# Kernel optimization log

Hardware: AMD Instinct MI355X
Metric: run time of the kernel (lower is better)

Reference implementation:

```python
import jax, jax.numpy as jnp
import numpy as np

B, C, N, T = 16, 32, 300, 12
ST, DH, CO = 40, 16, 32
DY_INTERVAL = 3
GDEP = 2
ALPHA = 0.05


def setup_inputs() -> dict:
    key = jax.random.key(0)
    ks = jax.random.split(key, 12)
    w = lambda k, shape, s=0.1: (jax.random.normal(k, shape, jnp.float32) * s)
    return {
        "x": jax.random.normal(ks[0], (B, C, N, T), jnp.float32),
        "st_node_fea": jax.random.normal(ks[1], (N, ST), jnp.float32),
        "W_s2d": w(ks[2], (ST, DH)), "b_s2d": jnp.zeros((DH,), jnp.float32),
        "W_rz": w(ks[3], (C + DH, 2 * DH)), "b_rz": jnp.zeros((2 * DH,), jnp.float32),
        "W_h": w(ks[4], (C + DH, DH)), "b_h": jnp.zeros((DH,), jnp.float32),
        "W_c1_fc2": w(ks[5], (2 * DH, DH)), "b_c1_fc2": jnp.zeros((DH,), jnp.float32),
        "W_c1_fc1": w(ks[6], (DH, 1)), "b_c1_fc1": jnp.zeros((1,), jnp.float32),
        "W_c2_fc2": w(ks[7], (2 * DH, DH)), "b_c2_fc2": jnp.zeros((DH,), jnp.float32),
        "W_c2_fc1": w(ks[8], (DH, 1)), "b_c2_fc1": jnp.zeros((1,), jnp.float32),
        "W_mlp": w(ks[9], ((GDEP + 1) * C, CO)), "b_mlp": jnp.zeros((CO,), jnp.float32),
    }


def _edge_score(hs, W_fc2, b_fc2, W_fc1, b_fc1):
    # normal_conv: fc1(relu(fc2(concat([sent, revi], -1)))).
    # fc2 over concat is decomposed into two halves to avoid the [B,N,N,2*DH] concat.
    dh = hs.shape[-1]
    Wa, Wb = W_fc2[:dh], W_fc2[dh:]
    h = jax.nn.relu((hs @ Wa)[:, :, None, :] + (hs @ Wb)[:, None, :, :] + b_fc2)  # [B,N,N,DH]
    return (h @ W_fc1 + b_fc1)[..., 0]  # [B,N,N]


def reference(x, st_node_fea, W_s2d, b_s2d, W_rz, b_rz, W_h, b_h,
              W_c1_fc2, b_c1_fc2, W_c1_fc1, b_c1_fc1,
              W_c2_fc2, b_c2_fc2, W_c2_fc1, b_c2_fc1, W_mlp, b_mlp):
    b, c, n, t = x.shape
    nc = t // DY_INTERVAL
    states0 = jnp.broadcast_to((st_node_fea @ W_s2d + b_s2d)[None], (b, n, DH)) + 0.0
    chunks = jnp.moveaxis(x.reshape(b, c, n, nc, DY_INTERVAL), 3, 0)  # [nc,B,C,N,di]

    def step(states, x_i):
        # GRU-style dynamic graph learner
        inp = jnp.mean(x_i, axis=-1).transpose(0, 2, 1)  # [B,N,C]
        cat = jnp.concatenate([inp, states], -1)
        rz = jax.nn.sigmoid(cat @ W_rz + b_rz)
        r, z = jnp.split(rz, 2, axis=-1)
        h_ = jnp.tanh(jnp.concatenate([inp, r * states], -1) @ W_h + b_h)
        new_state = z * states + (1.0 - z) * h_
        hs = jax.nn.relu(new_state)  # [B,N,DH]
        support = _edge_score(hs, W_c1_fc2, b_c1_fc2, W_c1_fc1, b_c1_fc1)
        mask = _edge_score(hs, W_c2_fc2, b_c2_fc2, W_c2_fc1, b_c2_fc1)
        adj = support * jax.nn.sigmoid(mask)  # [B,N,N]
        # MixProp multi-hop graph conv
        h = x_i
        outs = [h]
        for _ in range(GDEP):
            h = ALPHA * x_i + (1.0 - ALPHA) * jnp.einsum('bcwt,bvw->bcvt', h, adj)
            outs.append(h)
        ho = jnp.concatenate(outs, axis=1)  # [B,(GDEP+1)*C,N,di]
        out = jnp.einsum('bcnt,co->bont', ho, W_mlp) + b_mlp[None, :, None, None]
        return new_state, out

    _, outs = jax.lax.scan(step, states0, chunks)  # [nc,B,CO,N,di]
    return jnp.moveaxis(outs, 0, 3).reshape(b, W_mlp.shape[1], n, t)
```

## Files before the change

kernel.cpp:

```cpp
#include <hip/hip_runtime.h>
#include <hip/hip_bf16.h>
#include <math.h>

#define BB 16
#define CC 32
#define NN 300
#define TT 12
#define STF 40
#define DHD 16
#define COO 32
#define NCH 4
#define COL 96
#define NIB 64
#define KP  320
#define ALPHAF 0.05f

typedef __attribute__((ext_vector_type(8))) short short8;
typedef __attribute__((ext_vector_type(4))) float f32x4;

#define O_INP   0
#define O_XT    614400
#define O_GA1   2457600
#define O_GB1   2764800
#define O_GA2   3072000
#define O_GB2   3379200
#define O_ADJB  3686400
#define O_XTB   6963200
#define O_H1B   7946240

__device__ __forceinline__ float sigf(float x){ return 1.0f/(1.0f+expf(-x)); }

__global__ void k_prep(const float* __restrict__ x, float* __restrict__ xt,
                       __hip_bfloat16* __restrict__ xtb, float* __restrict__ inp){
    int idx = blockIdx.x*256 + threadIdx.x;
    if (idx >= BB*CC*NN) return;
    int n = idx % NN;
    int c = (idx / NN) % CC;
    int b = idx / (NN*CC);
    const float* xp = x + ((b*CC + c)*NN + n)*TT;
    float v[TT];
    #pragma unroll
    for (int t=0;t<TT;t++) v[t] = xp[t];
    #pragma unroll
    for (int i=0;i<NCH;i++){
        float m = (v[3*i]+v[3*i+1]+v[3*i+2])*(1.0f/3.0f);
        int ib = i*BB + b;
        inp[((size_t)ib*NN + n)*CC + c] = m;
        #pragma unroll
        for (int t=0;t<3;t++){
            float val = v[3*i+t];
            int col = c*3 + t;
            xt [((size_t)ib*NN + n)*COL + col] = val;
            xtb[((size_t)ib*COL + col)*KP + n] = __float2bfloat16(val);
        }
    }
}

__global__ void k_gru_all(const float* __restrict__ stnf, const float* __restrict__ W_s2d,
                          const float* __restrict__ b_s2d, const float* __restrict__ inp,
                          const float* __restrict__ W_rz, const float* __restrict__ b_rz,
                          const float* __restrict__ W_h,  const float* __restrict__ b_h,
                          const float* __restrict__ Wc1,  const float* __restrict__ Wc2,
                          float* __restrict__ ga1, float* __restrict__ gb1,
                          float* __restrict__ ga2, float* __restrict__ gb2){
    int row = blockIdx.x;
    int n   = row % NN;
    int tid = threadIdx.x;
    __shared__ float cat[48];
    __shared__ float r_s[16], z_s[16], hs_s[16], st_s[16];
    if (tid < 16){
        float acc = b_s2d[tid];
        const float* srow = stnf + n*STF;
        #pragma unroll
        for (int k=0;k<STF;k++) acc += srow[k]*W_s2d[k*DHD + tid];
        st_s[tid] = acc;
    }
    __syncthreads();
    for (int i=0;i<NCH;i++){
        const float* ip = inp + ((size_t)i*BB*NN + row)*CC;
        if (tid < CC) cat[tid] = ip[tid];
        else if (tid < 48) cat[tid] = st_s[tid-32];
        __syncthreads();
        if (tid < 32){
            float acc = b_rz[tid];
            #pragma unroll
            for (int k=0;k<48;k++) acc += cat[k]*W_rz[k*32 + tid];
            float s = sigf(acc);
            if (tid < 16) r_s[tid] = s; else z_s[tid-16] = s;
        }
        __syncthreads();
        if (tid < 16) cat[32+tid] = r_s[tid]*st_s[tid];
        __syncthreads();
        if (tid < 16){
            float acc = b_h[tid];
            #pragma unroll
            for (int k=0;k<48;k++) acc += cat[k]*W_h[k*DHD + tid];
            float h_ = tanhf(acc);
            float z  = z_s[tid];
            float ns = z*st_s[tid] + (1.0f-z)*h_;
            st_s[tid] = ns;
            hs_s[tid] = fmaxf(ns, 0.0f);
        }
        __syncthreads();
        int j = tid & 15, which = tid >> 4;
        const float* W = (which < 2) ? Wc1 : Wc2;
        int off = (which & 1) ? 16*DHD : 0;
        float acc = 0.0f;
        #pragma unroll
        for (int k=0;k<16;k++) acc += hs_s[k]*W[off + k*DHD + j];
        float* dst = (which==0)? ga1 : (which==1)? gb1 : (which==2)? ga2 : gb2;
        dst[((size_t)i*BB*NN + row)*DHD + j] = acc;
        __syncthreads();
    }
}

#define AVT 8
__global__ void k_adj(const float* __restrict__ ga1, const float* __restrict__ gb1,
                      const float* __restrict__ ga2, const float* __restrict__ gb2,
                      const float* __restrict__ bfc2_1, const float* __restrict__ wfc1_1, const float* __restrict__ bfc1_1,
                      const float* __restrict__ bfc2_2, const float* __restrict__ wfc1_2, const float* __restrict__ bfc1_2,
                      __hip_bfloat16* __restrict__ adjb){
    int tile = blockIdx.x % 38;
    int ib   = blockIdx.x / 38;
    int v0 = tile * AVT;
    int tid = threadIdx.x;
    __shared__ float a1[AVT][16], a2[AVT][16];
    __shared__ float w1[16], w2[16];
    if (tid < 16) w1[tid] = wfc1_1[tid];
    else if (tid < 32) w2[tid-16] = wfc1_2[tid-16];
    {
        int vl = tid >> 5, which = (tid >> 4) & 1, k = tid & 15;
        int v = v0 + vl;
        float val = 0.0f;
        if (v < NN)
            val = which ? (ga2[((size_t)ib*NN+v)*DHD + k] + bfc2_2[k])
                        : (ga1[((size_t)ib*NN+v)*DHD + k] + bfc2_1[k]);
        if (which) a2[vl][k] = val; else a1[vl][k] = val;
    }
    float B1 = bfc1_1[0], B2 = bfc1_2[0];
    __syncthreads();
    for (int w = tid; w < KP; w += 256){
        if (w < NN){
            const float4* p1 = (const float4*)(gb1 + ((size_t)ib*NN + w)*DHD);
            const float4* p2 = (const float4*)(gb2 + ((size_t)ib*NN + w)*DHD);
            float4 A[4], Bv[4];
            #pragma unroll
            for (int q=0;q<4;q++){ A[q]=p1[q]; Bv[q]=p2[q]; }
            const float* g1 = (const float*)A;
            const float* g2 = (const float*)Bv;
            for (int vl=0; vl<AVT; vl++){
                if (v0+vl >= NN) break;
                float s = B1, m = B2;
                #pragma unroll
                for (int k=0;k<16;k++){
                    s += fmaxf(a1[vl][k] + g1[k], 0.0f)*w1[k];
                    m += fmaxf(a2[vl][k] + g2[k], 0.0f)*w2[k];
                }
                adjb[((size_t)ib*KP + v0+vl)*KP + w] = __float2bfloat16(s * sigf(m));
            }
        } else {
            for (int vl=0; vl<AVT; vl++){
                if (v0+vl >= NN) break;
                adjb[((size_t)ib*KP + v0+vl)*KP + w] = __float2bfloat16(0.0f);
            }
        }
    }
}

__device__ __forceinline__ void conv_mfma_tile(const __hip_bfloat16* __restrict__ adjb,
                                               const __hip_bfloat16* __restrict__ Hb,
                                               int ib, int v0, int wave, int lane,
                                               f32x4& acc0, f32x4& acc1, f32x4& acc2){
    int l15 = lane & 15, lk = lane >> 4;
    int wrow = (wave & 1) * 16;
    int wcol = (wave >> 1) * 48;
    const short8* Ap  = (const short8*)(adjb + ((size_t)ib*KP + v0 + wrow + l15)*KP + 8*lk);
    const short8* Bp0 = (const short8*)(Hb   + ((size_t)ib*COL + wcol +  0 + l15)*KP + 8*lk);
    const short8* Bp1 = (const short8*)(Hb   + ((size_t)ib*COL + wcol + 16 + l15)*KP + 8*lk);
    const short8* Bp2 = (const short8*)(Hb   + ((size_t)ib*COL + wcol + 32 + l15)*KP + 8*lk);
    #pragma unroll 2
    for (int kk=0; kk<KP/32; kk++){
        short8 a = Ap[kk*4];
        acc0 = __builtin_amdgcn_mfma_f32_16x16x32_bf16(a, Bp0[kk*4], acc0, 0, 0, 0);
        acc1 = __builtin_amdgcn_mfma_f32_16x16x32_bf16(a, Bp1[kk*4], acc1, 0, 0, 0);
        acc2 = __builtin_amdgcn_mfma_f32_16x16x32_bf16(a, Bp2[kk*4], acc2, 0, 0, 0);
    }
}

__global__ __launch_bounds__(256) void k_conv1(const __hip_bfloat16* __restrict__ adjb,
                                               const __hip_bfloat16* __restrict__ xtb,
                                               const float* __restrict__ xt,
                                               __hip_bfloat16* __restrict__ h1b){
    int ib = blockIdx.x / 10;
    int v0 = (blockIdx.x % 10) * 32;
    int tid = threadIdx.x;
    int wave = tid >> 6, lane = tid & 63;
    int l15 = lane & 15, lk = lane >> 4;
    int wrow = (wave & 1) * 16;
    int wcol = (wave >> 1) * 48;
    __shared__ float hbuf[COL][33];
    f32x4 acc0 = {0.f,0.f,0.f,0.f}, acc1 = acc0, acc2 = acc0;
    conv_mfma_tile(adjb, xtb, ib, v0, wave, lane, acc0, acc1, acc2);
    f32x4 accs[3] = {acc0, acc1, acc2};
    #pragma unroll
    for (int t=0;t<3;t++){
        int col = wcol + t*16 + l15;
        #pragma unroll
        for (int r=0;r<4;r++){
            int vloc = wrow + lk*4 + r;
            int v = v0 + vloc;
            float xval = (v < NN) ? xt[((size_t)ib*NN + v)*COL + col] : 0.0f;
            hbuf[col][vloc] = ALPHAF*xval + (1.0f-ALPHAF)*accs[t][r];
        }
    }
    __syncthreads();
    for (int idx = tid; idx < COL*32; idx += 256){
        int col = idx >> 5, vloc = idx & 31;
        int v = v0 + vloc;
        if (v < NN)
            h1b[((size_t)ib*COL + col)*KP + v] = __float2bfloat16(hbuf[col][vloc]);
    }
}

__global__ __launch_bounds__(256) void k_conv2_mlp(const __hip_bfloat16* __restrict__ adjb,
                                                   const __hip_bfloat16* __restrict__ h1b,
                                                   const float* __restrict__ xt,
                                                   const float* __restrict__ Wm,
                                                   const float* __restrict__ bmlp,
                                                   float* __restrict__ out){
    int ib = blockIdx.x / 10;
    int v0 = (blockIdx.x % 10) * 32;
    int b  = ib % BB, chunk = ib / BB;
    int tid = threadIdx.x;
    int wave = tid >> 6, lane = tid & 63;
    int l15 = lane & 15, lk = lane >> 4;
    int wrow = (wave & 1) * 16;
    int wcol = (wave >> 1) * 48;
    __shared__ float hs[3][COL][33];
    f32x4 acc0 = {0.f,0.f,0.f,0.f}, acc1 = acc0, acc2 = acc0;
    conv_mfma_tile(adjb, h1b, ib, v0, wave, lane, acc0, acc1, acc2);
    f32x4 accs[3] = {acc0, acc1, acc2};
    #pragma unroll
    for (int t=0;t<3;t++){
        int col = wcol + t*16 + l15;
        #pragma unroll
        for (int r=0;r<4;r++){
            int vloc = wrow + lk*4 + r;
            int v = v0 + vloc;
            float xval = (v < NN) ? xt[((size_t)ib*NN + v)*COL + col] : 0.0f;
            hs[2][col][vloc] = ALPHAF*xval + (1.0f-ALPHAF)*accs[t][r];
        }
    }
    for (int idx = tid; idx < 32*COL; idx += 256){
        int vloc = idx / COL, col = idx % COL;
        int v = v0 + vloc;
        hs[0][col][vloc] = (v < NN) ? xt[((size_t)ib*NN + v)*COL + col] : 0.0f;
    }
    for (int idx = tid; idx < COL*32; idx += 256){
        int col = idx >> 5, vloc = idx & 31;
        int v = v0 + vloc;
        hs[1][col][vloc] = (v < NN) ? __bfloat162float(h1b[((size_t)ib*COL + col)*KP + v]) : 0.0f;
    }
    __syncthreads();
    for (int e = tid; e < COO*32*3; e += 256){
        int o  = e / 96;
        int r  = e % 96;
        int vl = r / 3, t = r % 3;
        int v = v0 + vl;
        if (v >= NN) continue;
        float acc = bmlp[o];
        #pragma unroll
        for (int c=0;c<CC;c++){
            int col = c*3 + t;
            acc += hs[0][col][vl]*Wm[c*COO + o]
                 + hs[1][col][vl]*Wm[(CC+c)*COO + o]
                 + hs[2][col][vl]*Wm[(2*CC+c)*COO + o];
        }
        out[(((size_t)b*COO + o)*NN + v)*TT + chunk*3 + t] = acc;
    }
}

extern "C" void kernel_launch(void* const* d_in, const int* in_sizes, int n_in,
                              void* d_out, int out_size, void* d_ws, size_t ws_size,
                              hipStream_t stream){
    const float* x     = (const float*)d_in[0];
    const float* stnf  = (const float*)d_in[1];
    const float* W_s2d = (const float*)d_in[2];
    const float* b_s2d = (const float*)d_in[3];
    const float* W_rz  = (const float*)d_in[4];
    const float* b_rz  = (const float*)d_in[5];
    const float* W_h   = (const float*)d_in[6];
    const float* b_h   = (const float*)d_in[7];
    const float* Wc1f2 = (const float*)d_in[8];
    const float* bc1f2 = (const float*)d_in[9];
    const float* Wc1f1 = (const float*)d_in[10];
    const float* bc1f1 = (const float*)d_in[11];
    const float* Wc2f2 = (const float*)d_in[12];
    const float* bc2f2 = (const float*)d_in[13];
    const float* Wc2f1 = (const float*)d_in[14];
    const float* bc2f1 = (const float*)d_in[15];
    const float* W_mlp = (const float*)d_in[16];
    const float* b_mlp = (const float*)d_in[17];
    float* out = (float*)d_out;
    float* ws  = (float*)d_ws;

    float* inp = ws + O_INP;
    float* xt  = ws + O_XT;
    float* ga1 = ws + O_GA1;
    float* gb1 = ws + O_GB1;
    float* ga2 = ws + O_GA2;
    float* gb2 = ws + O_GB2;
    __hip_bfloat16* adjb = (__hip_bfloat16*)(ws + O_ADJB);
    __hip_bfloat16* xtb  = (__hip_bfloat16*)(ws + O_XTB);
    __hip_bfloat16* h1b  = (__hip_bfloat16*)(ws + O_H1B);

    hipLaunchKernelGGL(k_prep, dim3(600), dim3(256), 0, stream, x, xt, xtb, inp);
    hipLaunchKernelGGL(k_gru_all, dim3(BB*NN), dim3(64), 0, stream,
                       stnf, W_s2d, b_s2d, inp, W_rz, b_rz, W_h, b_h, Wc1f2, Wc2f2,
                       ga1, gb1, ga2, gb2);
    hipLaunchKernelGGL(k_adj, dim3(NIB*38), dim3(256), 0, stream,
                       ga1, gb1, ga2, gb2,
                       bc1f2, Wc1f1, bc1f1, bc2f2, Wc2f1, bc2f1, adjb);
    hipLaunchKernelGGL(k_conv1, dim3(NIB*10), dim3(256), 0, stream,
                       adjb, xtb, xt, h1b);
    hipLaunchKernelGGL(k_conv2_mlp, dim3(NIB*10), dim3(256), 0, stream,
                       adjb, h1b, xt, W_mlp, b_mlp, out);
}
```

Baseline: 255.0 us.

## Run the MixProp MLP on bf16 MFMA and store x/h1 as bf16

Replaces the scalar fp32 MLP loop in k_conv2_mlp with bf16 16x16x32 MFMA tiles. It reads x, h1 and a transposed bf16 W_mlp staged in LDS in a [t][hop][v][c] layout. The fp32 xt buffer becomes a bf16 node-major copy, and conv1 also writes a node-major h1 copy so conv2 can load it with coalesced reads. k_prep now zero-fills the KP padding of xtb and h1b. The aim is lower ALU time and less memory traffic, at the cost of extra bf16 rounding on the x and MLP inputs.

```diff
diff --git a/kernel.cpp b/kernel.cpp
--- a/kernel.cpp
+++ b/kernel.cpp
@@ -14,26 +14,44 @@
 #define NIB 64
 #define KP  320
 #define ALPHAF 0.05f
+#define HS 40
 
 typedef __attribute__((ext_vector_type(8))) short short8;
 typedef __attribute__((ext_vector_type(4))) float f32x4;
+typedef unsigned short ushort_t;
 
 #define O_INP   0
-#define O_XT    614400
-#define O_GA1   2457600
-#define O_GB1   2764800
-#define O_GA2   3072000
-#define O_GB2   3379200
-#define O_ADJB  3686400
-#define O_XTB   6963200
-#define O_H1B   7946240
+#define O_XVB   614400
+#define O_GA1   1536000
+#define O_GB1   1843200
+#define O_GA2   2150400
+#define O_GB2   2457600
+#define O_ADJB  2764800
+#define O_XTB   6041600
+#define O_H1B   7024640
+#define O_H1VB  8007680
+#define O_WMB   8929280
 
 __device__ __forceinline__ float sigf(float x){ return 1.0f/(1.0f+expf(-x)); }
 
-__global__ void k_prep(const float* __restrict__ x, float* __restrict__ xt,
-                       __hip_bfloat16* __restrict__ xtb, float* __restrict__ inp){
+__global__ void k_prep(const float* __restrict__ x, __hip_bfloat16* __restrict__ xtb,
+                       __hip_bfloat16* __restrict__ xvb, float* __restrict__ inp,
+                       __hip_bfloat16* __restrict__ h1b, const float* __restrict__ Wm,
+                       __hip_bfloat16* __restrict__ Wmb){
     int idx = blockIdx.x*256 + threadIdx.x;
     if (idx >= BB*CC*NN) return;
+    if (idx < NIB*COL*(KP-NN)){
+        int kk  = idx % (KP-NN);
+        int col = (idx / (KP-NN)) % COL;
+        int ib  = idx / ((KP-NN)*COL);
+        size_t off = ((size_t)ib*COL + col)*KP + NN + kk;
+        xtb[off] = __float2bfloat16(0.0f);
+        h1b[off] = __float2bfloat16(0.0f);
+    }
+    if (idx < COO*COL){
+        int o = idx / COL, k = idx % COL;
+        Wmb[o*COL + k] = __float2bfloat16(Wm[k*COO + o]);
+    }
     int n = idx % NN;
     int c = (idx / NN) % CC;
     int b = idx / (NN*CC);
@@ -50,8 +68,8 @@
         for (int t=0;t<3;t++){
             float val = v[3*i+t];
             int col = c*3 + t;
-            xt [((size_t)ib*NN + n)*COL + col] = val;
             xtb[((size_t)ib*COL + col)*KP + n] = __float2bfloat16(val);
+            xvb[((size_t)ib*NN + n)*COL + col] = __float2bfloat16(val);
         }
     }
 }
@@ -189,8 +207,9 @@
 
 __global__ __launch_bounds__(256) void k_conv1(const __hip_bfloat16* __restrict__ adjb,
                                                const __hip_bfloat16* __restrict__ xtb,
-                                               const float* __restrict__ xt,
-                                               __hip_bfloat16* __restrict__ h1b){
+                                               const __hip_bfloat16* __restrict__ xvb,
+                                               __hip_bfloat16* __restrict__ h1b,
+                                               __hip_bfloat16* __restrict__ h1vb){
     int ib = blockIdx.x / 10;
     int v0 = (blockIdx.x % 10) * 32;
     int tid = threadIdx.x;
@@ -209,7 +228,7 @@
         for (int r=0;r<4;r++){
             int vloc = wrow + lk*4 + r;
             int v = v0 + vloc;
-            float xval = (v < NN) ? xt[((size_t)ib*NN + v)*COL + col] : 0.0f;
+            float xval = (v < NN) ? __bfloat162float(xvb[((size_t)ib*NN + v)*COL + col]) : 0.0f;
             hbuf[col][vloc] = ALPHAF*xval + (1.0f-ALPHAF)*accs[t][r];
         }
     }
@@ -220,12 +239,19 @@
         if (v < NN)
             h1b[((size_t)ib*COL + col)*KP + v] = __float2bfloat16(hbuf[col][vloc]);
     }
+    for (int idx = tid; idx < 32*COL; idx += 256){
+        int vloc = idx / COL, col = idx % COL;
+        int v = v0 + vloc;
+        if (v < NN)
+            h1vb[((size_t)ib*NN + v)*COL + col] = __float2bfloat16(hbuf[col][vloc]);
+    }
 }
 
 __global__ __launch_bounds__(256) void k_conv2_mlp(const __hip_bfloat16* __restrict__ adjb,
                                                    const __hip_bfloat16* __restrict__ h1b,
-                                                   const float* __restrict__ xt,
-                                                   const float* __restrict__ Wm,
+                                                   const __hip_bfloat16* __restrict__ xvb,
+                                                   const __hip_bfloat16* __restrict__ h1vb,
+                                                   const __hip_bfloat16* __restrict__ Wmb,
                                                    const float* __restrict__ bmlp,
                                                    float* __restrict__ out){
     int ib = blockIdx.x / 10;
@@ -236,47 +262,62 @@
     int l15 = lane & 15, lk = lane >> 4;
     int wrow = (wave & 1) * 16;
     int wcol = (wave >> 1) * 48;
-    __shared__ float hs[3][COL][33];
+    __shared__ ushort_t hst[3][3][32][HS];
+    for (int idx = tid; idx < 2*32*COL; idx += 256){
+        int which = idx / (32*COL);
+        int r     = idx % (32*COL);
+        int vloc  = r / COL, col = r % COL;
+        int v = v0 + vloc;
+        int c = col/3, t = col%3;
+        ushort_t val = 0;
+        if (v < NN){
+            const ushort_t* src = (const ushort_t*)(which ? h1vb : xvb);
+            val = src[((size_t)ib*NN + v)*COL + col];
+        }
+        hst[t][which][vloc][c] = val;
+    }
     f32x4 acc0 = {0.f,0.f,0.f,0.f}, acc1 = acc0, acc2 = acc0;
     conv_mfma_tile(adjb, h1b, ib, v0, wave, lane, acc0, acc1, acc2);
     f32x4 accs[3] = {acc0, acc1, acc2};
     #pragma unroll
-    for (int t=0;t<3;t++){
-        int col = wcol + t*16 + l15;
+    for (int tt=0;tt<3;tt++){
+        int col = wcol + tt*16 + l15;
+        int c = col/3, t = col%3;
         #pragma unroll
         for (int r=0;r<4;r++){
             int vloc = wrow + lk*4 + r;
             int v = v0 + vloc;
-            float xval = (v < NN) ? xt[((size_t)ib*NN + v)*COL + col] : 0.0f;
-            hs[2][col][vloc] = ALPHAF*xval + (1.0f-ALPHAF)*accs[t][r];
-        }
-    }
-    for (int idx = tid; idx < 32*COL; idx += 256){
-        int vloc = idx / COL, col = idx % COL;
-        int v = v0 + vloc;
-        hs[0][col][vloc] = (v < NN) ? xt[((size_t)ib*NN + v)*COL + col] : 0.0f;
-    }
-    for (int idx = tid; idx < COL*32; idx += 256){
-        int col = idx >> 5, vloc = idx & 31;
-        int v = v0 + vloc;
-        hs[1][col][vloc] = (v < NN) ? __bfloat162float(h1b[((size_t)ib*COL + col)*KP + v]) : 0.0f;
+            float val = 0.0f;
+            if (v < NN){
+                float xval = __bfloat162float(xvb[((size_t)ib*NN + v)*COL + col]);
+                val = ALPHAF*xval + (1.0f-ALPHAF)*accs[tt][r];
+            }
+            __hip_bfloat16 bv = __float2bfloat16(val);
+            hst[t][2][vloc][c] = *(ushort_t*)&bv;
+        }
     }
     __syncthreads();
-    for (int e = tid; e < COO*32*3; e += 256){
-        int o  = e / 96;
-        int r  = e % 96;
-        int vl = r / 3, t = r % 3;
-        int v = v0 + vl;
-        if (v >= NN) continue;
-        float acc = bmlp[o];
-        #pragma unroll
-        for (int c=0;c<CC;c++){
-            int col = c*3 + t;
-            acc += hs[0][col][vl]*Wm[c*COO + o]
-                 + hs[1][col][vl]*Wm[(CC+c)*COO + o]
-                 + hs[2][col][vl]*Wm[(2*CC+c)*COO + o];
-        }
-        out[(((size_t)b*COO + o)*NN + v)*TT + chunk*3 + t] = acc;
+    #pragma unroll
+    for (int j=0;j<3;j++){
+        int tile = wave + 4*j;
+        int t  = tile >> 2;
+        int vt = (tile & 3) >> 1;
+        int ot = tile & 1;
+        f32x4 acc = {0.f,0.f,0.f,0.f};
+        #pragma unroll
+        for (int d=0;d<3;d++){
+            short8 a = *(const short8*)&hst[t][d][vt*16 + l15][8*lk];
+            short8 bfr = *(const short8*)(Wmb + ((size_t)(ot*16 + l15))*COL + d*32 + 8*lk);
+            acc = __builtin_amdgcn_mfma_f32_16x16x32_bf16(a, bfr, acc, 0, 0, 0);
+        }
+        int o = ot*16 + l15;
+        float bias = bmlp[o];
+        #pragma unroll
+        for (int r=0;r<4;r++){
+            int v = v0 + vt*16 + lk*4 + r;
+            if (v < NN)
+                out[(((size_t)b*COO + o)*NN + v)*TT + chunk*3 + t] = acc[r] + bias;
+        }
     }
 }
 
@@ -305,16 +346,18 @@
     float* ws  = (float*)d_ws;
 
     float* inp = ws + O_INP;
-    float* xt  = ws + O_XT;
     float* ga1 = ws + O_GA1;
     float* gb1 = ws + O_GB1;
     float* ga2 = ws + O_GA2;
     float* gb2 = ws + O_GB2;
+    __hip_bfloat16* xvb  = (__hip_bfloat16*)(ws + O_XVB);
     __hip_bfloat16* adjb = (__hip_bfloat16*)(ws + O_ADJB);
     __hip_bfloat16* xtb  = (__hip_bfloat16*)(ws + O_XTB);
     __hip_bfloat16* h1b  = (__hip_bfloat16*)(ws + O_H1B);
-
-    hipLaunchKernelGGL(k_prep, dim3(600), dim3(256), 0, stream, x, xt, xtb, inp);
+    __hip_bfloat16* h1vb = (__hip_bfloat16*)(ws + O_H1VB);
+    __hip_bfloat16* Wmb  = (__hip_bfloat16*)(ws + O_WMB);
+
+    hipLaunchKernelGGL(k_prep, dim3(600), dim3(256), 0, stream, x, xtb, xvb, inp, h1b, W_mlp, Wmb);
     hipLaunchKernelGGL(k_gru_all, dim3(BB*NN), dim3(64), 0, stream,
                        stnf, W_s2d, b_s2d, inp, W_rz, b_rz, W_h, b_h, Wc1f2, Wc2f2,
                        ga1, gb1, ga2, gb2);
@@ -322,7 +365,7 @@
                        ga1, gb1, ga2, gb2,
                        bc1f2, Wc1f1, bc1f1, bc2f2, Wc2f1, bc2f1, adjb);
     hipLaunchKernelGGL(k_conv1, dim3(NIB*10), dim3(256), 0, stream,
-                       adjb, xtb, xt, h1b);
+                       adjb, xtb, xvb, h1b, h1vb);
     hipLaunchKernelGGL(k_conv2_mlp, dim3(NIB*10), dim3(256), 0, stream,
-                       adjb, h1b, xt, W_mlp, b_mlp, out);
-}
+                       adjb, h1b, xvb, h1vb, Wmb, b_mlp, out);
+}
```

Measured after the change: 223.5 us. 12.3% less time.
